# Kernel tuning notes

Measured on AMD Instinct MI355X. Metric: run time of the kernel, lower is better.

Reference implementation:

```python
import jax, jax.numpy as jnp
import numpy as np

N = 50000      # nodes
E = 800000     # edges (avg degree 16)
IN = 128       # input_dim
HID = 64       # hidden_dim
HEADS = 2      # heads in layer 1
OUT = 32       # output_dim
NEG_SLOPE = 0.2


def setup_inputs() -> dict:
    key = jax.random.key(0)
    ks = jax.random.split(key, 8)
    s = 0.1
    x = jax.random.normal(ks[0], (N, IN), jnp.float32)
    edge_index = jax.random.randint(ks[1], (2, E), 0, N, dtype=jnp.int64)
    W1 = jax.random.normal(ks[2], (IN, HEADS * HID), jnp.float32) * s
    att_src1 = jax.random.normal(ks[3], (HEADS, HID), jnp.float32) * s
    att_dst1 = jax.random.normal(ks[4], (HEADS, HID), jnp.float32) * s
    bias1 = jnp.zeros((HEADS * HID,), jnp.float32)
    W2 = jax.random.normal(ks[5], (HEADS * HID, OUT), jnp.float32) * s
    att_src2 = jax.random.normal(ks[6], (1, OUT), jnp.float32) * s
    att_dst2 = jax.random.normal(ks[7], (1, OUT), jnp.float32) * s
    bias2 = jnp.zeros((OUT,), jnp.float32)
    return {"x": x, "edge_index": edge_index,
            "W1": W1, "att_src1": att_src1, "att_dst1": att_dst1, "bias1": bias1,
            "W2": W2, "att_src2": att_src2, "att_dst2": att_dst2, "bias2": bias2}


def gat_conv(x, src, dst, W, a_src, a_dst, bias, heads, out_ch, concat):
    # PyG GATConv: linear -> per-node attn terms -> per-edge LeakyReLU score
    # -> segment softmax over incoming edges of each dst -> weighted scatter-sum.
    n = x.shape[0]
    h = (x @ W).reshape(n, heads, out_ch)                 # [N,H,C]
    a_s = jnp.einsum('nhc,hc->nh', h, a_src)              # [N,H]
    a_d = jnp.einsum('nhc,hc->nh', h, a_dst)              # [N,H]
    e = jax.nn.leaky_relu(a_s[src] + a_d[dst], NEG_SLOPE) # [E,H]
    e_max = jax.ops.segment_max(e, dst, num_segments=n)   # [N,H] (self-loops => no empty segment)
    ex = jnp.exp(e - e_max[dst])
    denom = jax.ops.segment_sum(ex, dst, num_segments=n)
    alpha = ex / denom[dst]                               # [E,H]
    msg = h[src] * alpha[..., None]                       # [E,H,C]
    out = jax.ops.segment_sum(msg, dst, num_segments=n)   # [N,H,C]
    out = out.reshape(n, heads * out_ch) if concat else out.mean(axis=1)
    return out + bias


def reference(x, edge_index, W1, att_src1, att_dst1, bias1, W2, att_src2, att_dst2, bias2):
    # add self-loops (PyG default add_self_loops=True)
    loops = jnp.arange(N, dtype=edge_index.dtype)
    src = jnp.concatenate([edge_index[0], loops])
    dst = jnp.concatenate([edge_index[1], loops])
    h = gat_conv(x, src, dst, W1, att_src1, att_dst1, bias1, HEADS, HID, True)
    h = jax.nn.elu(h)
    out = gat_conv(h, src, dst, W2, att_src2, att_dst2, bias2, 1, OUT, False)
    return out
```

## Files before the change

### kernel.cpp

```cpp
#include <hip/hip_runtime.h>
#include <hip/hip_bf16.h>
#include <math.h>

#define NN 50000
#define EE 800000
#define NEG 0.2f
#define BKT 64
#define G1_BLKS 782
#define FILL_BLKS 782

#define OFF_H1B    0UL
#define OFF_H2B    (OFF_H1B + (size_t)NN*128*2)
#define OFF_ASAD1  (OFF_H2B + (size_t)NN*32*2)
#define OFF_ASAD2  (OFF_ASAD1 + (size_t)NN*4*4)
#define OFF_CUR    (OFF_ASAD2 + (size_t)NN*2*4)
#define OFF_BKT    (OFF_CUR + (size_t)NN*4)
#define OFF_FLAG   (OFF_BKT + (size_t)NN*BKT*2 + 256)

__device__ __forceinline__ unsigned short f2bf(float f) {
    unsigned u = __float_as_uint(f);
    unsigned r = (u + 0x7fffu + ((u >> 16) & 1u)) >> 16;
    return (unsigned short)r;
}
__device__ __forceinline__ float bflo(unsigned v) { return __uint_as_float(v << 16); }
__device__ __forceinline__ float bfhi(unsigned v) { return __uint_as_float(v & 0xffff0000u); }

__global__ void k_detect(const int* __restrict__ p, int* __restrict__ flag) {
    int t = threadIdx.x;
    int v = p[2*t + 1];
    unsigned long long b = __ballot(v != 0);
    if (t == 0) flag[0] = (b == 0ULL) ? 1 : 0;
}

__global__ __launch_bounds__(256) void k_build_gemm1(
        const int* __restrict__ raw, const int* __restrict__ flag,
        int* __restrict__ cur, unsigned short* __restrict__ bkt,
        const float* __restrict__ x, const float* __restrict__ W,
        const float* __restrict__ atts, const float* __restrict__ attd,
        unsigned short* __restrict__ h1b, float* __restrict__ asad) {
    __shared__ float Wl[32*128];
    __shared__ float xs[32*76];
    int t = threadIdx.x;

    if (blockIdx.x >= G1_BLKS) {
        int bid = blockIdx.x - G1_BLKS;
        int f = flag[0];
        int base = bid*1024 + t;
        int s[4], d[4]; bool act[4];
        #pragma unroll
        for (int u = 0; u < 4; ++u) {
            int i = base + 256*u;
            act[u] = i < EE;
            int ii = act[u] ? i : 0;
            if (f) { s[u] = raw[2*ii]; d[u] = raw[2*(EE + ii)]; }
            else   { s[u] = raw[ii];   d[u] = raw[EE + ii]; }
        }
        #pragma unroll
        for (int u = 0; u < 4; ++u) {
            if (act[u]) {
                int pos = atomicAdd(&cur[d[u]], 1);
                if (pos < BKT) bkt[(size_t)d[u]*BKT + pos] = (unsigned short)s[u];
            }
        }
        return;
    }

    int bid = blockIdx.x;
    int cg = t & 31, ng = t >> 5;
    int j0 = cg * 4;
    int nb = bid * 64;
    const float4* W4 = (const float4*)W;
    const float4* x4 = (const float4*)x;

    float4 a0={0,0,0,0},a1={0,0,0,0},a2={0,0,0,0},a3={0,0,0,0};
    float4 a4={0,0,0,0},a5={0,0,0,0},a6={0,0,0,0},a7={0,0,0,0};

    for (int k0 = 0; k0 < 128; k0 += 32) {
        __syncthreads();
        #pragma unroll
        for (int i = t; i < 1024; i += 256) {
            int kk = i >> 5, c4 = i & 31;
            *(float4*)&Wl[kk*128 + c4*4] = W4[(size_t)(k0+kk)*32 + c4];
        }
        #pragma unroll
        for (int i = t; i < 512; i += 256) {
            int row = i >> 3, c4 = i & 7;
            float4 v = make_float4(0.f,0.f,0.f,0.f);
            int n = nb + row;
            if (n < NN) v = x4[(size_t)n*32 + (k0>>2) + c4];
            xs[(c4*4+0)*76 + row] = v.x;
            xs[(c4*4+1)*76 + row] = v.y;
            xs[(c4*4+2)*76 + row] = v.z;
            xs[(c4*4+3)*76 + row] = v.w;
        }
        __syncthreads();
        #pragma unroll
        for (int kk = 0; kk < 32; ++kk) {
            float4 w = *(const float4*)&Wl[kk*128 + j0];
            float4 xa = *(const float4*)&xs[kk*76 + ng*8];
            float4 xb = *(const float4*)&xs[kk*76 + ng*8 + 4];
            a0.x += xa.x*w.x; a0.y += xa.x*w.y; a0.z += xa.x*w.z; a0.w += xa.x*w.w;
            a1.x += xa.y*w.x; a1.y += xa.y*w.y; a1.z += xa.y*w.z; a1.w += xa.y*w.w;
            a2.x += xa.z*w.x; a2.y += xa.z*w.y; a2.z += xa.z*w.z; a2.w += xa.z*w.w;
            a3.x += xa.w*w.x; a3.y += xa.w*w.y; a3.z += xa.w*w.z; a3.w += xa.w*w.w;
            a4.x += xb.x*w.x; a4.y += xb.x*w.y; a4.z += xb.x*w.z; a4.w += xb.x*w.w;
            a5.x += xb.y*w.x; a5.y += xb.y*w.y; a5.z += xb.y*w.z; a5.w += xb.y*w.w;
            a6.x += xb.z*w.x; a6.y += xb.z*w.y; a6.z += xb.z*w.z; a6.w += xb.z*w.w;
            a7.x += xb.w*w.x; a7.y += xb.w*w.y; a7.z += xb.w*w.z; a7.w += xb.w*w.w;
        }
    }
    int head = cg >> 4;
    int cb = (cg & 15) * 4;
    float4 s4 = *(const float4*)&atts[head*64 + cb];
    float4 d4 = *(const float4*)&attd[head*64 + cb];
    #define EPI(ai, m) { \
        int n = nb + ng*8 + m; \
        if (n < NN) { \
            ushort4 pk; pk.x = f2bf(ai.x); pk.y = f2bf(ai.y); pk.z = f2bf(ai.z); pk.w = f2bf(ai.w); \
            *(ushort4*)&h1b[(size_t)n*128 + j0] = pk; \
            float ps = ai.x*s4.x + ai.y*s4.y + ai.z*s4.z + ai.w*s4.w; \
            float pd = ai.x*d4.x + ai.y*d4.y + ai.z*d4.z + ai.w*d4.w; \
            ps += __shfl_xor(ps, 1, 64); pd += __shfl_xor(pd, 1, 64); \
            ps += __shfl_xor(ps, 2, 64); pd += __shfl_xor(pd, 2, 64); \
            ps += __shfl_xor(ps, 4, 64); pd += __shfl_xor(pd, 4, 64); \
            ps += __shfl_xor(ps, 8, 64); pd += __shfl_xor(pd, 8, 64); \
            if ((cg & 15) == 0) { asad[(size_t)n*4 + head] = ps; asad[(size_t)n*4 + 2 + head] = pd; } \
        } }
    EPI(a0,0) EPI(a1,1) EPI(a2,2) EPI(a3,3) EPI(a4,4) EPI(a5,5) EPI(a6,6) EPI(a7,7)
    #undef EPI
}

__global__ __launch_bounds__(256) void k_agg1f(const uint4* __restrict__ h1q, const float* __restrict__ asad,
                       const int* __restrict__ cur, const unsigned short* __restrict__ bkt,
                       const float* __restrict__ bias,
                       const float* __restrict__ atts2, const float* __restrict__ attd2,
                       const float* __restrict__ W2,
                       unsigned short* __restrict__ h2b, float* __restrict__ asad2) {
    __shared__ float W2l[128*32];
    __shared__ float hrow[4][128];
    int t = threadIdx.x;
    int lane = t & 63, wid = t >> 6;
    for (int i = t; i < 1024; i += 256) ((float4*)W2l)[i] = ((const float4*)W2)[i];

    int n = blockIdx.x*4 + wid;
    n = __builtin_amdgcn_readfirstlane(n);
    int cnt = cur[n]; cnt = cnt < BKT ? cnt : BKT;
    int tot = cnt + 1;
    int q = lane >> 4, c = lane & 15;
    float ad0 = asad[(size_t)n*4 + 2], ad1 = asad[(size_t)n*4 + 3];
    bool head1 = c >= 8;
    const unsigned short* row = bkt + (size_t)n*BKT;
    float den = 0.f;
    float a0=0.f,a1=0.f,a2=0.f,a3=0.f,a4=0.f,a5=0.f,a6=0.f,a7=0.f;
    for (int i = 0; i < tot; i += 16) {
        int i0 = i+q, i1 = i+4+q, i2 = i+8+q, i3 = i+12+q;
        int r0 = (int)row[i0 & 63], r1 = (int)row[i1 & 63];
        int r2 = (int)row[i2 & 63], r3 = (int)row[i3 & 63];
        int s0 = (i0 < cnt) ? r0 : n, s1 = (i1 < cnt) ? r1 : n;
        int s2 = (i2 < cnt) ? r2 : n, s3 = (i3 < cnt) ? r3 : n;
        bool ac0 = i0 < tot, ac1 = i1 < tot, ac2 = i2 < tot, ac3 = i3 < tot;
        float2 w0 = *(const float2*)&asad[(size_t)s0*4];
        float2 w1 = *(const float2*)&asad[(size_t)s1*4];
        float2 w2 = *(const float2*)&asad[(size_t)s2*4];
        float2 w3 = *(const float2*)&asad[(size_t)s3*4];
        uint4 p0 = h1q[(size_t)s0*16 + c];
        uint4 p1 = h1q[(size_t)s1*16 + c];
        uint4 p2 = h1q[(size_t)s2*16 + c];
        uint4 p3 = h1q[(size_t)s3*16 + c];
        #define SCORE(wv, ac) ({ \
            float e0 = wv.x + ad0; e0 = (e0 > 0.f) ? e0 : NEG*e0; \
            float e1 = wv.y + ad1; e1 = (e1 > 0.f) ? e1 : NEG*e1; \
            float ex = __expf(head1 ? e1 : e0); if (!(ac)) ex = 0.f; ex; })
        float x0 = SCORE(w0, ac0), x1 = SCORE(w1, ac1);
        float x2 = SCORE(w2, ac2), x3 = SCORE(w3, ac3);
        #undef SCORE
        den += (x0 + x1) + (x2 + x3);
        a0 += x0*bflo(p0.x) + x1*bflo(p1.x) + x2*bflo(p2.x) + x3*bflo(p3.x);
        a1 += x0*bfhi(p0.x) + x1*bfhi(p1.x) + x2*bfhi(p2.x) + x3*bfhi(p3.x);
        a2 += x0*bflo(p0.y) + x1*bflo(p1.y) + x2*bflo(p2.y) + x3*bflo(p3.y);
        a3 += x0*bfhi(p0.y) + x1*bfhi(p1.y) + x2*bfhi(p2.y) + x3*bfhi(p3.y);
        a4 += x0*bflo(p0.z) + x1*bflo(p1.z) + x2*bflo(p2.z) + x3*bflo(p3.z);
        a5 += x0*bfhi(p0.z) + x1*bfhi(p1.z) + x2*bfhi(p2.z) + x3*bfhi(p3.z);
        a6 += x0*bflo(p0.w) + x1*bflo(p1.w) + x2*bflo(p2.w) + x3*bflo(p3.w);
        a7 += x0*bfhi(p0.w) + x1*bfhi(p1.w) + x2*bfhi(p2.w) + x3*bfhi(p3.w);
    }
    #define RED(v) v += __shfl_xor(v, 16, 64); v += __shfl_xor(v, 32, 64);
    RED(den) RED(a0) RED(a1) RED(a2) RED(a3) RED(a4) RED(a5) RED(a6) RED(a7)
    #undef RED
    {
        float4 b0 = *(const float4*)&bias[c*8];
        float4 b1 = *(const float4*)&bias[c*8 + 4];
        float r = 1.f / den;
        a0 = a0*r + b0.x; a1 = a1*r + b0.y; a2 = a2*r + b0.z; a3 = a3*r + b0.w;
        a4 = a4*r + b1.x; a5 = a5*r + b1.y; a6 = a6*r + b1.z; a7 = a7*r + b1.w;
        a0 = (a0 > 0.f) ? a0 : expm1f(a0); a1 = (a1 > 0.f) ? a1 : expm1f(a1);
        a2 = (a2 > 0.f) ? a2 : expm1f(a2); a3 = (a3 > 0.f) ? a3 : expm1f(a3);
        a4 = (a4 > 0.f) ? a4 : expm1f(a4); a5 = (a5 > 0.f) ? a5 : expm1f(a5);
        a6 = (a6 > 0.f) ? a6 : expm1f(a6); a7 = (a7 > 0.f) ? a7 : expm1f(a7);
        if (q == 0) {
            float4 v0 = {a0,a1,a2,a3}, v1 = {a4,a5,a6,a7};
            *(float4*)&hrow[wid][c*8] = v0;
            *(float4*)&hrow[wid][c*8 + 4] = v1;
        }
    }
    __syncthreads();
    {
        int j = lane & 31;
        int kbase = (lane >> 5) * 64;
        float acc0 = 0.f, acc1 = 0.f, acc2 = 0.f, acc3 = 0.f;
        const float* hr = hrow[wid];
        #pragma unroll
        for (int k4 = 0; k4 < 16; k4 += 4) {
            float4 h0 = *(const float4*)&hr[kbase + k4*4];
            float4 h1v = *(const float4*)&hr[kbase + k4*4 + 4];
            float4 h2v = *(const float4*)&hr[kbase + k4*4 + 8];
            float4 h3v = *(const float4*)&hr[kbase + k4*4 + 12];
            acc0 += h0.x*W2l[(kbase+k4*4+0)*32+j]  + h0.y*W2l[(kbase+k4*4+1)*32+j]
                  + h0.z*W2l[(kbase+k4*4+2)*32+j]  + h0.w*W2l[(kbase+k4*4+3)*32+j];
            acc1 += h1v.x*W2l[(kbase+k4*4+4)*32+j] + h1v.y*W2l[(kbase+k4*4+5)*32+j]
                  + h1v.z*W2l[(kbase+k4*4+6)*32+j] + h1v.w*W2l[(kbase+k4*4+7)*32+j];
            acc2 += h2v.x*W2l[(kbase+k4*4+8)*32+j] + h2v.y*W2l[(kbase+k4*4+9)*32+j]
                  + h2v.z*W2l[(kbase+k4*4+10)*32+j]+ h2v.w*W2l[(kbase+k4*4+11)*32+j];
            acc3 += h3v.x*W2l[(kbase+k4*4+12)*32+j]+ h3v.y*W2l[(kbase+k4*4+13)*32+j]
                  + h3v.z*W2l[(kbase+k4*4+14)*32+j]+ h3v.w*W2l[(kbase+k4*4+15)*32+j];
        }
        float acc = (acc0 + acc1) + (acc2 + acc3);
        acc += __shfl_xor(acc, 32, 64);
        float ps = acc * atts2[j];
        float pd = acc * attd2[j];
        ps += __shfl_xor(ps, 1, 64); pd += __shfl_xor(pd, 1, 64);
        ps += __shfl_xor(ps, 2, 64); pd += __shfl_xor(pd, 2, 64);
        ps += __shfl_xor(ps, 4, 64); pd += __shfl_xor(pd, 4, 64);
        ps += __shfl_xor(ps, 8, 64); pd += __shfl_xor(pd, 8, 64);
        ps += __shfl_xor(ps, 16, 64); pd += __shfl_xor(pd, 16, 64);
        if (lane < 32) h2b[(size_t)n*32 + j] = f2bf(acc);
        if (lane == 0) { asad2[(size_t)n*2] = ps; asad2[(size_t)n*2 + 1] = pd; }
    }
}

__global__ __launch_bounds__(256) void k_agg2(const unsigned* __restrict__ h2u, const float* __restrict__ asad2,
                       const int* __restrict__ cur, const unsigned short* __restrict__ bkt,
                       const float* __restrict__ bias, float* __restrict__ out) {
    int lane = threadIdx.x & 63;
    int n = blockIdx.x*4 + (threadIdx.x >> 6);
    n = __builtin_amdgcn_readfirstlane(n);
    int cnt = cur[n]; cnt = cnt < BKT ? cnt : BKT;
    int tot = cnt + 1;
    int q = lane >> 4, c = lane & 15;
    float ad = asad2[(size_t)n*2 + 1];
    const unsigned short* row = bkt + (size_t)n*BKT;
    float den = 0.f, aA = 0.f, aB = 0.f;
    for (int i = 0; i < tot; i += 16) {
        int i0 = i+q, i1 = i+4+q, i2 = i+8+q, i3 = i+12+q;
        int r0 = (int)row[i0 & 63], r1 = (int)row[i1 & 63];
        int r2 = (int)row[i2 & 63], r3 = (int)row[i3 & 63];
        int s0 = (i0 < cnt) ? r0 : n, s1 = (i1 < cnt) ? r1 : n;
        int s2 = (i2 < cnt) ? r2 : n, s3 = (i3 < cnt) ? r3 : n;
        bool ac0 = i0 < tot, ac1 = i1 < tot, ac2 = i2 < tot, ac3 = i3 < tot;
        float e0 = asad2[(size_t)s0*2] + ad; e0 = (e0 > 0.f) ? e0 : NEG*e0;
        float e1 = asad2[(size_t)s1*2] + ad; e1 = (e1 > 0.f) ? e1 : NEG*e1;
        float e2 = asad2[(size_t)s2*2] + ad; e2 = (e2 > 0.f) ? e2 : NEG*e2;
        float e3 = asad2[(size_t)s3*2] + ad; e3 = (e3 > 0.f) ? e3 : NEG*e3;
        unsigned p0 = h2u[(size_t)s0*16 + c];
        unsigned p1 = h2u[(size_t)s1*16 + c];
        unsigned p2 = h2u[(size_t)s2*16 + c];
        unsigned p3 = h2u[(size_t)s3*16 + c];
        float x0 = __expf(e0); if (!ac0) x0 = 0.f;
        float x1 = __expf(e1); if (!ac1) x1 = 0.f;
        float x2 = __expf(e2); if (!ac2) x2 = 0.f;
        float x3 = __expf(e3); if (!ac3) x3 = 0.f;
        den += (x0 + x1) + (x2 + x3);
        aA += x0*bflo(p0) + x1*bflo(p1) + x2*bflo(p2) + x3*bflo(p3);
        aB += x0*bfhi(p0) + x1*bfhi(p1) + x2*bfhi(p2) + x3*bfhi(p3);
    }
    #define RED(v) v += __shfl_xor(v, 16, 64); v += __shfl_xor(v, 32, 64);
    RED(den) RED(aA) RED(aB)
    #undef RED
    if (q == 0) {
        float2 bb = ((const float2*)bias)[c];
        float r = 1.f / den;
        float2 ov; ov.x = aA*r + bb.x; ov.y = aB*r + bb.y;
        ((float2*)out)[(size_t)n*16 + c] = ov;
    }
}

extern "C" void kernel_launch(void* const* d_in, const int* in_sizes, int n_in,
                              void* d_out, int out_size, void* d_ws, size_t ws_size,
                              hipStream_t stream) {
    (void)in_sizes; (void)n_in; (void)out_size; (void)ws_size;
    const float* x   = (const float*)d_in[0];
    const int*   er  = (const int*)d_in[1];
    const float* W1  = (const float*)d_in[2];
    const float* as1 = (const float*)d_in[3];
    const float* ad1 = (const float*)d_in[4];
    const float* b1  = (const float*)d_in[5];
    const float* W2  = (const float*)d_in[6];
    const float* as2 = (const float*)d_in[7];
    const float* ad2 = (const float*)d_in[8];
    const float* b2  = (const float*)d_in[9];
    float* out = (float*)d_out;
    char* ws = (char*)d_ws;

    unsigned short* h1b = (unsigned short*)(ws + OFF_H1B);
    unsigned short* h2b = (unsigned short*)(ws + OFF_H2B);
    float* asad1 = (float*)(ws + OFF_ASAD1);
    float* asd2  = (float*)(ws + OFF_ASAD2);
    int*   cur   = (int*)(ws + OFF_CUR);
    unsigned short* bkt = (unsigned short*)(ws + OFF_BKT);
    int*   flag  = (int*)(ws + OFF_FLAG);

    hipMemsetAsync(ws + OFF_CUR, 0, (size_t)NN*4, stream);
    k_detect<<<1, 64, 0, stream>>>(er, flag);
    k_build_gemm1<<<G1_BLKS + FILL_BLKS, 256, 0, stream>>>(er, flag, cur, bkt,
                                                           x, W1, as1, ad1, h1b, asad1);
    k_agg1f<<<NN/4, 256, 0, stream>>>((const uint4*)h1b, asad1, cur, bkt, b1,
                                      as2, ad2, W2, h2b, asd2);
    k_agg2<<<NN/4, 256, 0, stream>>>((const unsigned*)h2b, asd2, cur, bkt, b2, out);
}
```

Before: 223.8 us.

## Compute layer-2 projection from registers using transposed W2, dropping LDS staging and barrier

The layer-2 linear projection in the aggregation kernel now uses each lane's aggregated registers directly against a pre-transposed W2 read from global memory or cache. This removes the per-block copy of W2 into shared memory, the shared hidden-row buffer and the __syncthreads. A small pre-kernel transposes W2 alongside the edge-format detection. Separately, each bucket-fill block now handles twice as many edges, halving the fill block count. The projection trades LDS traffic for extra cross-lane shuffles and global W2 loads.

```diff
diff --git a/kernel.cpp b/kernel.cpp
--- a/kernel.cpp
+++ b/kernel.cpp
@@ -7,7 +7,7 @@
 #define NEG 0.2f
 #define BKT 64
 #define G1_BLKS 782
-#define FILL_BLKS 782
+#define FILL_BLKS 391
 
 #define OFF_H1B    0UL
 #define OFF_H2B    (OFF_H1B + (size_t)NN*128*2)
@@ -16,20 +16,29 @@
 #define OFF_CUR    (OFF_ASAD2 + (size_t)NN*2*4)
 #define OFF_BKT    (OFF_CUR + (size_t)NN*4)
 #define OFF_FLAG   (OFF_BKT + (size_t)NN*BKT*2 + 256)
+#define OFF_W2T    (OFF_FLAG + 256)
 
 __device__ __forceinline__ unsigned short f2bf(float f) {
     unsigned u = __float_as_uint(f);
     unsigned r = (u + 0x7fffu + ((u >> 16) & 1u)) >> 16;
     return (unsigned short)r;
 }
+__device__ __forceinline__ unsigned pack2(float lo, float hi) {
+    return (unsigned)f2bf(lo) | ((unsigned)f2bf(hi) << 16);
+}
 __device__ __forceinline__ float bflo(unsigned v) { return __uint_as_float(v << 16); }
 __device__ __forceinline__ float bfhi(unsigned v) { return __uint_as_float(v & 0xffff0000u); }
 
-__global__ void k_detect(const int* __restrict__ p, int* __restrict__ flag) {
-    int t = threadIdx.x;
-    int v = p[2*t + 1];
-    unsigned long long b = __ballot(v != 0);
-    if (t == 0) flag[0] = (b == 0ULL) ? 1 : 0;
+__global__ void k_pre(const int* __restrict__ p, int* __restrict__ flag,
+                      const float* __restrict__ W2, float* __restrict__ W2T) {
+    int t = threadIdx.x, b = blockIdx.x;
+    if (b == 0 && t < 64) {
+        int v = p[2*t + 1];
+        unsigned long long bm = __ballot(v != 0);
+        if (t == 0) flag[0] = (bm == 0ULL) ? 1 : 0;
+    }
+    int i = b*256 + t;
+    if (i < 4096) { int k = i >> 5, j = i & 31; W2T[j*128 + k] = W2[i]; }
 }
 
 __global__ __launch_bounds__(256) void k_build_gemm1(
@@ -45,10 +54,10 @@
     if (blockIdx.x >= G1_BLKS) {
         int bid = blockIdx.x - G1_BLKS;
         int f = flag[0];
-        int base = bid*1024 + t;
-        int s[4], d[4]; bool act[4];
-        #pragma unroll
-        for (int u = 0; u < 4; ++u) {
+        int base = bid*2048 + t;
+        int s[8], d[8]; bool act[8];
+        #pragma unroll
+        for (int u = 0; u < 8; ++u) {
             int i = base + 256*u;
             act[u] = i < EE;
             int ii = act[u] ? i : 0;
@@ -56,7 +65,7 @@
             else   { s[u] = raw[ii];   d[u] = raw[EE + ii]; }
         }
         #pragma unroll
-        for (int u = 0; u < 4; ++u) {
+        for (int u = 0; u < 8; ++u) {
             if (act[u]) {
                 int pos = atomicAdd(&cur[d[u]], 1);
                 if (pos < BKT) bkt[(size_t)d[u]*BKT + pos] = (unsigned short)s[u];
@@ -134,14 +143,10 @@
                        const int* __restrict__ cur, const unsigned short* __restrict__ bkt,
                        const float* __restrict__ bias,
                        const float* __restrict__ atts2, const float* __restrict__ attd2,
-                       const float* __restrict__ W2,
+                       const float* __restrict__ W2T,
                        unsigned short* __restrict__ h2b, float* __restrict__ asad2) {
-    __shared__ float W2l[128*32];
-    __shared__ float hrow[4][128];
     int t = threadIdx.x;
     int lane = t & 63, wid = t >> 6;
-    for (int i = t; i < 1024; i += 256) ((float4*)W2l)[i] = ((const float4*)W2)[i];
-
     int n = blockIdx.x*4 + wid;
     n = __builtin_amdgcn_readfirstlane(n);
     int cnt = cur[n]; cnt = cnt < BKT ? cnt : BKT;
@@ -197,43 +202,40 @@
         a2 = (a2 > 0.f) ? a2 : expm1f(a2); a3 = (a3 > 0.f) ? a3 : expm1f(a3);
         a4 = (a4 > 0.f) ? a4 : expm1f(a4); a5 = (a5 > 0.f) ? a5 : expm1f(a5);
         a6 = (a6 > 0.f) ? a6 : expm1f(a6); a7 = (a7 > 0.f) ? a7 : expm1f(a7);
-        if (q == 0) {
-            float4 v0 = {a0,a1,a2,a3}, v1 = {a4,a5,a6,a7};
-            *(float4*)&hrow[wid][c*8] = v0;
-            *(float4*)&hrow[wid][c*8 + 4] = v1;
-        }
-    }
-    __syncthreads();
+    }
+    float p0,p1,p2,p3,p4,p5,p6,p7;
     {
-        int j = lane & 31;
-        int kbase = (lane >> 5) * 64;
-        float acc0 = 0.f, acc1 = 0.f, acc2 = 0.f, acc3 = 0.f;
-        const float* hr = hrow[wid];
-        #pragma unroll
-        for (int k4 = 0; k4 < 16; k4 += 4) {
-            float4 h0 = *(const float4*)&hr[kbase + k4*4];
-            float4 h1v = *(const float4*)&hr[kbase + k4*4 + 4];
-            float4 h2v = *(const float4*)&hr[kbase + k4*4 + 8];
-            float4 h3v = *(const float4*)&hr[kbase + k4*4 + 12];
-            acc0 += h0.x*W2l[(kbase+k4*4+0)*32+j]  + h0.y*W2l[(kbase+k4*4+1)*32+j]
-                  + h0.z*W2l[(kbase+k4*4+2)*32+j]  + h0.w*W2l[(kbase+k4*4+3)*32+j];
-            acc1 += h1v.x*W2l[(kbase+k4*4+4)*32+j] + h1v.y*W2l[(kbase+k4*4+5)*32+j]
-                  + h1v.z*W2l[(kbase+k4*4+6)*32+j] + h1v.w*W2l[(kbase+k4*4+7)*32+j];
-            acc2 += h2v.x*W2l[(kbase+k4*4+8)*32+j] + h2v.y*W2l[(kbase+k4*4+9)*32+j]
-                  + h2v.z*W2l[(kbase+k4*4+10)*32+j]+ h2v.w*W2l[(kbase+k4*4+11)*32+j];
-            acc3 += h3v.x*W2l[(kbase+k4*4+12)*32+j]+ h3v.y*W2l[(kbase+k4*4+13)*32+j]
-                  + h3v.z*W2l[(kbase+k4*4+14)*32+j]+ h3v.w*W2l[(kbase+k4*4+15)*32+j];
-        }
-        float acc = (acc0 + acc1) + (acc2 + acc3);
-        acc += __shfl_xor(acc, 32, 64);
-        float ps = acc * atts2[j];
-        float pd = acc * attd2[j];
-        ps += __shfl_xor(ps, 1, 64); pd += __shfl_xor(pd, 1, 64);
-        ps += __shfl_xor(ps, 2, 64); pd += __shfl_xor(pd, 2, 64);
-        ps += __shfl_xor(ps, 4, 64); pd += __shfl_xor(pd, 4, 64);
-        ps += __shfl_xor(ps, 8, 64); pd += __shfl_xor(pd, 8, 64);
+        const float* wb = W2T + (size_t)(q*8)*128 + c*8;
+        #define DOT(jj) ({ \
+            float4 wA = *(const float4*)(wb + jj*128); \
+            float4 wB = *(const float4*)(wb + jj*128 + 4); \
+            (a0*wA.x + a1*wA.y + a2*wA.z + a3*wA.w) + \
+            (a4*wB.x + a5*wB.y + a6*wB.z + a7*wB.w); })
+        p0 = DOT(0); p1 = DOT(1); p2 = DOT(2); p3 = DOT(3);
+        p4 = DOT(4); p5 = DOT(5); p6 = DOT(6); p7 = DOT(7);
+        #undef DOT
+    }
+    #define RQ(v) v += __shfl_xor(v, 1, 64); v += __shfl_xor(v, 2, 64); \
+                  v += __shfl_xor(v, 4, 64); v += __shfl_xor(v, 8, 64);
+    RQ(p0) RQ(p1) RQ(p2) RQ(p3) RQ(p4) RQ(p5) RQ(p6) RQ(p7)
+    #undef RQ
+    if (c == 0) {
+        uint4 pk;
+        pk.x = pack2(p0, p1); pk.y = pack2(p2, p3);
+        pk.z = pack2(p4, p5); pk.w = pack2(p6, p7);
+        *(uint4*)&h2b[(size_t)n*32 + q*8] = pk;
+    }
+    {
+        float4 sA = *(const float4*)&atts2[q*8];
+        float4 sB = *(const float4*)&atts2[q*8 + 4];
+        float4 dA = *(const float4*)&attd2[q*8];
+        float4 dB = *(const float4*)&attd2[q*8 + 4];
+        float ps = (p0*sA.x + p1*sA.y + p2*sA.z + p3*sA.w)
+                 + (p4*sB.x + p5*sB.y + p6*sB.z + p7*sB.w);
+        float pd = (p0*dA.x + p1*dA.y + p2*dA.z + p3*dA.w)
+                 + (p4*dB.x + p5*dB.y + p6*dB.z + p7*dB.w);
         ps += __shfl_xor(ps, 16, 64); pd += __shfl_xor(pd, 16, 64);
-        if (lane < 32) h2b[(size_t)n*32 + j] = f2bf(acc);
+        ps += __shfl_xor(ps, 32, 64); pd += __shfl_xor(pd, 32, 64);
         if (lane == 0) { asad2[(size_t)n*2] = ps; asad2[(size_t)n*2 + 1] = pd; }
     }
 }
@@ -308,12 +310,13 @@
     int*   cur   = (int*)(ws + OFF_CUR);
     unsigned short* bkt = (unsigned short*)(ws + OFF_BKT);
     int*   flag  = (int*)(ws + OFF_FLAG);
+    float* W2T   = (float*)(ws + OFF_W2T);
 
     hipMemsetAsync(ws + OFF_CUR, 0, (size_t)NN*4, stream);
-    k_detect<<<1, 64, 0, stream>>>(er, flag);
+    k_pre<<<16, 256, 0, stream>>>(er, flag, W2, W2T);
     k_build_gemm1<<<G1_BLKS + FILL_BLKS, 256, 0, stream>>>(er, flag, cur, bkt,
                                                            x, W1, as1, ad1, h1b, asad1);
     k_agg1f<<<NN/4, 256, 0, stream>>>((const uint4*)h1b, asad1, cur, bkt, b1,
-                                      as2, ad2, W2, h2b, asd2);
+                                      as2, ad2, W2T, h2b, asd2);
     k_agg2<<<NN/4, 256, 0, stream>>>((const unsigned*)h2b, asd2, cur, bkt, b2, out);
 }
```

Result: faster. 218.2 us (-2.5%).
